# Performance work log

Hardware: AMD Instinct MI355X
Metric: run time of the kernel (lower is better)

## Reference

```python
import jax, jax.numpy as jnp
import numpy as np

# Dims: N tokens, top_k K, E experts, d_model D, expert hidden H
N, K, E, D, H = 4096, 2, 8, 1024, 1024


def setup_inputs() -> dict:
    key = jax.random.key(0)
    k1, k2, k3, k4, k5, k6 = jax.random.split(key, 6)
    x = jax.random.normal(k1, (N, D), dtype=jnp.float32)
    expert_indices = jax.random.randint(k2, (N, K), 0, E, dtype=jnp.int32)
    ew = jax.random.uniform(k3, (N, K), dtype=jnp.float32)
    expert_weights = ew / ew.sum(-1, keepdims=True)  # router probs over top-k
    # histogram consistent with expert_indices (computed by the router in the real model)
    batch_size_per_expert = jnp.bincount(expert_indices.reshape(-1), length=E).astype(jnp.int32)
    w1 = jax.random.normal(k4, (E, D, H), dtype=jnp.float32) * (D ** -0.5)
    w3 = jax.random.normal(k5, (E, D, H), dtype=jnp.float32) * (D ** -0.5)
    w2 = jax.random.normal(k6, (E, H, D), dtype=jnp.float32) * (H ** -0.5)
    return {
        "x": x,
        "expert_weights": expert_weights,
        "expert_indices": expert_indices,
        "batch_size_per_expert": batch_size_per_expert,
        "w1": w1,
        "w2": w2,
        "w3": w3,
    }


def reference(x, expert_weights, expert_indices, batch_size_per_expert, w1, w2, w3):
    """Dropless MoE: sort token-copies by expert, grouped-GEMM SwiGLU, unpermute+combine."""
    nk = N * K
    flat_idx = expert_indices.reshape(nk)               # (N*K,)
    order = jnp.argsort(flat_idx)                        # stable sort -> permutation into expert order
    x_perm = x[order // K]                               # (N*K, D) gather source token per copy
    gs = batch_size_per_expert.astype(jnp.int32)         # grouped-GEMM group sizes, sums to N*K
    # per-expert SwiGLU MLP via grouped GEMM (rows of x_perm are contiguous per expert)
    h = jax.nn.silu(jax.lax.ragged_dot(x_perm, w1, gs)) * jax.lax.ragged_dot(x_perm, w3, gs)  # (N*K, H)
    out_perm = jax.lax.ragged_dot(h, w2, gs)             # (N*K, D)
    # unpermute: scatter rows back to original (token, k) order
    out_flat = jnp.zeros_like(x_perm).at[order].set(out_perm)  # (N*K, D)
    # weighted combine over top-k copies
    out = jnp.einsum("nk,nkd->nd", expert_weights, out_flat.reshape(N, K, D))
    return out
```

## Files before the change

### kernel.cpp

```cpp
#include <hip/hip_runtime.h>
#include <hip/hip_bf16.h>
#include <stdint.h>

#define N_TOK   4096
#define TOPK    2
#define N_EXP   8
#define D_MODEL 1024
#define H_DIM   1024
#define NK      (N_TOK * TOPK)
#define MAX_TILES 72

typedef __attribute__((ext_vector_type(8))) short bf16x8;
typedef __attribute__((ext_vector_type(4))) float f32x4;
typedef __attribute__((ext_vector_type(4))) unsigned int uint32x4;
typedef __attribute__((ext_vector_type(2))) unsigned int uint32x2;
typedef unsigned short bfbits;

__device__ inline bfbits f2bf_bits(float f) {
  union { float f; unsigned int u; } v; v.f = f;
  unsigned int r = v.u + 0x7FFFu + ((v.u >> 16) & 1u);
  return (bfbits)(r >> 16);
}
__device__ inline float bf2f(unsigned short u) {
  union { unsigned int u; float f; } v; v.u = ((unsigned int)u) << 16;
  return v.f;
}

__device__ inline void glds16(const bfbits* g, bfbits* l) {
  __builtin_amdgcn_global_load_lds(
      (const __attribute__((address_space(1))) void*)g,
      (__attribute__((address_space(3))) void*)l, 16, 0, 0);
}

__global__ __launch_bounds__(256, 4) void prepass_kernel(
    const float* __restrict__ x, const int* __restrict__ eidx,
    const int* __restrict__ bspe,
    const float* __restrict__ w1, const float* __restrict__ w2,
    const float* __restrict__ w3,
    bfbits* __restrict__ w1t, bfbits* __restrict__ w2t,
    bfbits* __restrict__ w3t, bfbits* __restrict__ xb,
    int* __restrict__ meta, int* __restrict__ row_src,
    int* __restrict__ pos_of) {
  int z = blockIdx.z;
  int tid = threadIdx.x;

  if (z >= 1 && z <= 24) {
    int zz = z - 1;
    const size_t MAT = (size_t)1024 * 1024;
    const float* src; bfbits* dst;
    if (zz < 8)       { src = w1 + (size_t)zz * MAT;        dst = w1t + (size_t)zz * MAT; }
    else if (zz < 16) { src = w3 + (size_t)(zz - 8) * MAT;  dst = w3t + (size_t)(zz - 8) * MAT; }
    else              { src = w2 + (size_t)(zz - 16) * MAT; dst = w2t + (size_t)(zz - 16) * MAT; }

    __shared__ __align__(16) bfbits Ts[64 * 132];
    char* tsb = (char*)Ts;

    int r0 = blockIdx.y * 128, c0 = blockIdx.x * 64;
    int k = tid & 15, qw = tid >> 4;
    int c = k * 4;

    float4 v0[4], v1[4];
#pragma unroll
    for (int it = 0; it < 4; it++) {
      int r = it * 32 + qw * 2;
      v0[it] = *(const float4*)&src[(size_t)(r0 + r) * 1024 + c0 + c];
      v1[it] = *(const float4*)&src[(size_t)(r0 + r + 1) * 1024 + c0 + c];
    }
#pragma unroll
    for (int it = 0; it < 4; it++) {
      int r = it * 32 + qw * 2;
      const float* a0 = (const float*)&v0[it];
      const float* a1 = (const float*)&v1[it];
#pragma unroll
      for (int j = 0; j < 4; j++) {
        int a = c + j;
        int xo = ((a >> 4) & 3) << 3;
        unsigned int pk = (unsigned int)f2bf_bits(a0[j]) |
                          ((unsigned int)f2bf_bits(a1[j]) << 16);
        *(unsigned int*)(tsb + a * 264 + ((r * 2) ^ xo)) = pk;
      }
    }
    __syncthreads();
    int g = tid >> 3, m = tid & 7;
#pragma unroll
    for (int it2 = 0; it2 < 2; it2++) {
      int o = it2 * 32 + g;
      int base = o * 264;
      int xo = ((o >> 4) & 3) << 3;
      uint32x2 p0 = *(const uint32x2*)(tsb + base + ((m * 32 +  0) ^ xo));
      uint32x2 p1 = *(const uint32x2*)(tsb + base + ((m * 32 +  8) ^ xo));
      uint32x2 p2 = *(const uint32x2*)(tsb + base + ((m * 32 + 16) ^ xo));
      uint32x2 p3 = *(const uint32x2*)(tsb + base + ((m * 32 + 24) ^ xo));
      size_t ob = (size_t)(c0 + o) * 1024 + r0 + m * 16;
      uint32x4 s0; s0.x = p0.x; s0.y = p0.y; s0.z = p1.x; s0.w = p1.y;
      uint32x4 s1; s1.x = p2.x; s1.y = p2.y; s1.z = p3.x; s1.w = p3.y;
      *(uint32x4*)&dst[ob] = s0;
      *(uint32x4*)&dst[ob + 8] = s1;
    }
  } else if (z >= 25) {
    int idx = (z - 25) * 128 + blockIdx.y * 16 + blockIdx.x;
    const float4* xv = (const float4*)x;
    ushort4* xo = (ushort4*)xb;
#pragma unroll
    for (int q = 0; q < 4; q++) {
      int fi = idx * 1024 + q * 256 + tid;
      float4 v = xv[fi];
      ushort4 o;
      o.x = f2bf_bits(v.x); o.y = f2bf_bits(v.y);
      o.z = f2bf_bits(v.z); o.w = f2bf_bits(v.w);
      xo[fi] = o;
    }
  } else {
    if (blockIdx.x != 0 || blockIdx.y != 0) return;
    __shared__ int sm[162];
    __shared__ int scnt[N_EXP];
    if (tid == 0) {
      int acc = 0, nt = 0;
      for (int e = 0; e < N_EXP; e++) {
        sm[e] = acc;
        int g = bspe[e];
        for (int tt = 0; tt * 128 < g; tt++) {
          sm[18 + nt] = e;
          sm[90 + nt] = acc + tt * 128;
          nt++;
        }
        acc += g;
      }
      sm[8] = acc;
      sm[17] = nt;
      for (int i = nt; i < MAX_TILES; i++) { sm[18 + i] = 0; sm[90 + i] = 0; }
    }
    if (tid < N_EXP) scnt[tid] = 0;
    __syncthreads();
    int4 eb[8];
#pragma unroll
    for (int q = 0; q < 8; q++) eb[q] = ((const int4*)eidx)[q * 256 + tid];
#pragma unroll
    for (int q = 0; q < 8; q++) {
      int ii = (q * 256 + tid) * 4;
      const int* ev = (const int*)&eb[q];
#pragma unroll
      for (int j = 0; j < 4; j++) {
        int e = ev[j];
        int p = sm[e] + atomicAdd(&scnt[e], 1);
        row_src[p] = ii + j;
        pos_of[ii + j] = p;
      }
    }
    if (tid < 162) meta[tid] = sm[tid];
  }
}

__global__ __launch_bounds__(256, 3) void gemm_swiglu_kernel(
    const bfbits* __restrict__ xb, const bfbits* __restrict__ w1t,
    const bfbits* __restrict__ w3t, const int* __restrict__ row_src,
    const int* __restrict__ meta, bfbits* __restrict__ hb) {
  int nt = meta[17];
  int bt = blockIdx.y;
  if (bt >= nt) return;
  int e = meta[18 + bt];
  int row0 = meta[90 + bt];
  int rows_end = meta[e + 1];
  int n0 = blockIdx.x * 64;

  __shared__ __align__(16) bfbits As[128 * 64];
  __shared__ __align__(16) bfbits B1s[64 * 64];
  __shared__ __align__(16) bfbits B3s[64 * 64];

  int tid = threadIdx.x, lane = tid & 63, wv = tid >> 6;
  int r8 = lane >> 3, jl = lane & 7;
  int jg = jl ^ r8;

  const bfbits* gp[8]; bfbits* lp[8];
  for (int j = 0; j < 8; j++) {
    int s = wv * 8 + j;
    if (s < 16) {
      int tok = row_src[row0 + s * 8 + r8] >> 1;
      gp[j] = xb + (size_t)tok * D_MODEL + jg * 8;
      lp[j] = As + s * 512;
    } else if (s < 24) {
      int b = s - 16;
      gp[j] = w1t + ((size_t)e * H_DIM + n0 + b * 8 + r8) * D_MODEL + jg * 8;
      lp[j] = B1s + b * 512;
    } else {
      int b = s - 24;
      gp[j] = w3t + ((size_t)e * H_DIM + n0 + b * 8 + r8) * D_MODEL + jg * 8;
      lp[j] = B3s + b * 512;
    }
  }

  const f32x4 fzero = {0.f, 0.f, 0.f, 0.f};
  f32x4 accg[4][2], accu[4][2];
  for (int i = 0; i < 4; i++)
    for (int j = 0; j < 2; j++) { accg[i][j] = fzero; accu[i][j] = fzero; }

  int mw = (wv & 1) * 64, nwv = (wv >> 1) * 32;
  int qd = lane >> 4, lr = lane & 15, lr7 = lr & 7;

  for (int kk = 0; kk < D_MODEL / 64; kk++) {
    int ko = kk * 64;
    for (int j = 0; j < 8; j++) glds16(gp[j] + ko, lp[j]);
    __syncthreads();
    for (int ks = 0; ks < 2; ks++) {
      int sb = ((ks * 4 + qd) ^ lr7) << 3;
      bf16x8 af[4], b1f[2], b3f[2];
      for (int mi = 0; mi < 4; mi++)
        af[mi] = *(const bf16x8*)&As[(mw + mi * 16 + lr) * 64 + sb];
      for (int ni = 0; ni < 2; ni++) {
        b1f[ni] = *(const bf16x8*)&B1s[(nwv + ni * 16 + lr) * 64 + sb];
        b3f[ni] = *(const bf16x8*)&B3s[(nwv + ni * 16 + lr) * 64 + sb];
      }
      for (int mi = 0; mi < 4; mi++)
        for (int ni = 0; ni < 2; ni++) {
          accg[mi][ni] = __builtin_amdgcn_mfma_f32_16x16x32_bf16(af[mi], b1f[ni], accg[mi][ni], 0, 0, 0);
          accu[mi][ni] = __builtin_amdgcn_mfma_f32_16x16x32_bf16(af[mi], b3f[ni], accu[mi][ni], 0, 0, 0);
        }
    }
    __syncthreads();
  }

  for (int mi = 0; mi < 4; mi++) {
    int rbase = row0 + mw + mi * 16 + qd * 4;
    for (int r = 0; r < 4; r++) {
      int grow = rbase + r;
      if (grow < rows_end) {
        for (int ni = 0; ni < 2; ni++) {
          float gg = accg[mi][ni][r], u = accu[mi][ni][r];
          float h = gg / (1.f + __expf(-gg)) * u;
          hb[(size_t)grow * H_DIM + n0 + nwv + ni * 16 + lr] = f2bf_bits(h);
        }
      }
    }
  }
}

__global__ __launch_bounds__(256, 2) void gemm_out_kernel(
    const bfbits* __restrict__ hb, const bfbits* __restrict__ w2t,
    const int* __restrict__ meta, bfbits* __restrict__ out_perm) {
  int nt = meta[17];
  int bt = blockIdx.y;
  if (bt >= nt) return;
  int e = meta[18 + bt];
  int row0 = meta[90 + bt];
  int rows_end = meta[e + 1];
  int n0 = blockIdx.x * 128;

  __shared__ __align__(16) bfbits As[128 * 64];
  __shared__ __align__(16) bfbits Bs[128 * 64];

  int tid = threadIdx.x, lane = tid & 63, wv = tid >> 6;
  int r8 = lane >> 3, jl = lane & 7;
  int jg = jl ^ r8;

  const bfbits* gp[8]; bfbits* lp[8];
  for (int j = 0; j < 8; j++) {
    int s = wv * 8 + j;
    if (s < 16) {
      gp[j] = hb + (size_t)(row0 + s * 8 + r8) * H_DIM + jg * 8;
      lp[j] = As + s * 512;
    } else {
      int b = s - 16;
      gp[j] = w2t + ((size_t)e * D_MODEL + n0 + b * 8 + r8) * H_DIM + jg * 8;
      lp[j] = Bs + b * 512;
    }
  }

  const f32x4 fzero = {0.f, 0.f, 0.f, 0.f};
  f32x4 acc[4][4];
  for (int i = 0; i < 4; i++)
    for (int j = 0; j < 4; j++) acc[i][j] = fzero;

  int mw = (wv & 1) * 64, nw = (wv >> 1) * 64;
  int qd = lane >> 4, lr = lane & 15, lr7 = lr & 7;

  for (int kk = 0; kk < H_DIM / 64; kk++) {
    int ko = kk * 64;
    for (int j = 0; j < 8; j++) glds16(gp[j] + ko, lp[j]);
    __syncthreads();
    for (int ks = 0; ks < 2; ks++) {
      int sb = ((ks * 4 + qd) ^ lr7) << 3;
      bf16x8 af[4], bfr[4];
      for (int mi = 0; mi < 4; mi++)
        af[mi] = *(const bf16x8*)&As[(mw + mi * 16 + lr) * 64 + sb];
      for (int ni = 0; ni < 4; ni++)
        bfr[ni] = *(const bf16x8*)&Bs[(nw + ni * 16 + lr) * 64 + sb];
      for (int mi = 0; mi < 4; mi++)
        for (int ni = 0; ni < 4; ni++)
          acc[mi][ni] = __builtin_amdgcn_mfma_f32_16x16x32_bf16(af[mi], bfr[ni], acc[mi][ni], 0, 0, 0);
    }
    __syncthreads();
  }

  for (int mi = 0; mi < 4; mi++) {
    int rbase = row0 + mw + mi * 16 + qd * 4;
    for (int r = 0; r < 4; r++) {
      int grow = rbase + r;
      if (grow < rows_end) {
        for (int ni = 0; ni < 4; ni++)
          out_perm[(size_t)grow * D_MODEL + n0 + nw + ni * 16 + lr] = f2bf_bits(acc[mi][ni][r]);
      }
    }
  }
}

__global__ __launch_bounds__(256) void combine_kernel(
    const ushort4* __restrict__ out_perm, const int* __restrict__ pos_of,
    const float* __restrict__ ew, float4* __restrict__ out) {
  int tid = threadIdx.x;
#pragma unroll
  for (int q = 0; q < 4; q++) {
    int i = blockIdx.x * 1024 + q * 256 + tid;
    int tok = i >> 8;
    int col = i & 255;
    int p0 = pos_of[2 * tok], p1 = pos_of[2 * tok + 1];
    float w0 = ew[2 * tok], w1 = ew[2 * tok + 1];
    ushort4 a = out_perm[(size_t)p0 * 256 + col];
    ushort4 b = out_perm[(size_t)p1 * 256 + col];
    float4 o;
    o.x = w0 * bf2f(a.x) + w1 * bf2f(b.x);
    o.y = w0 * bf2f(a.y) + w1 * bf2f(b.y);
    o.z = w0 * bf2f(a.z) + w1 * bf2f(b.z);
    o.w = w0 * bf2f(a.w) + w1 * bf2f(b.w);
    out[i] = o;
  }
}

extern "C" void kernel_launch(void* const* d_in, const int* in_sizes, int n_in,
                              void* d_out, int out_size, void* d_ws, size_t ws_size,
                              hipStream_t stream) {
  const float* x  = (const float*)d_in[0];
  const float* ew = (const float*)d_in[1];
  const int* eidx = (const int*)d_in[2];
  const int* bspe = (const int*)d_in[3];
  const float* w1 = (const float*)d_in[4];
  const float* w2 = (const float*)d_in[5];
  const float* w3 = (const float*)d_in[6];
  float* out = (float*)d_out;

  char* ws = (char*)d_ws;
  const size_t MB = 1024 * 1024;
  bfbits* w1t   = (bfbits*)(ws);
  bfbits* w3t   = (bfbits*)(ws + 16 * MB);
  bfbits* w2t   = (bfbits*)(ws + 32 * MB);
  bfbits* xb    = (bfbits*)(ws + 48 * MB);
  bfbits* hb    = (bfbits*)(ws + 56 * MB);
  bfbits* out_perm = (bfbits*)(ws);
  int* row_src  = (int*)(ws + 72 * MB);
  int* pos_of   = (int*)(ws + 72 * MB + 32 * 1024);
  int* meta     = (int*)(ws + 72 * MB + 64 * 1024);

  prepass_kernel<<<dim3(16, 8, 33), 256, 0, stream>>>(
      x, eidx, bspe, w1, w2, w3, w1t, w2t, w3t, xb, meta, row_src, pos_of);
  gemm_swiglu_kernel<<<dim3(H_DIM / 64, MAX_TILES), 256, 0, stream>>>(
      xb, w1t, w3t, row_src, meta, hb);
  gemm_out_kernel<<<dim3(D_MODEL / 128, MAX_TILES), 256, 0, stream>>>(
      hb, w2t, meta, out_perm);
  combine_kernel<<<(N_TOK * D_MODEL / 4) / 1024, 256, 0, stream>>>(
      (const ushort4*)out_perm, pos_of, ew, (float4*)out);
}
```

Before: 240.1 us.

## Double-buffer LDS tiles in both expert GEMMs to overlap loads with MFMA

Both grouped-GEMM kernels switch from a single shared-memory tile to two ping-pong buffers. The global-to-LDS loads for the next K step are issued before the MFMAs on the current buffer, with an explicit vmcnt drain and barrier between steps. MFMA blocks are wrapped in s_setprio, and the inner loops are fully unrolled. This hides global load latency behind compute, but it doubles LDS use, so the SwiGLU kernel's launch bound drops from 3 to 2 blocks per CU and occupancy may fall.

```diff
diff --git a/kernel.cpp b/kernel.cpp
--- a/kernel.cpp
+++ b/kernel.cpp
@@ -31,6 +31,11 @@
       (const __attribute__((address_space(1))) void*)g,
       (__attribute__((address_space(3))) void*)l, 16, 0, 0);
 }
+
+#define DRAIN_BAR() do {                                   \
+    asm volatile("s_waitcnt vmcnt(0)" ::: "memory");       \
+    __builtin_amdgcn_s_barrier();                          \
+  } while (0)
 
 __global__ __launch_bounds__(256, 4) void prepass_kernel(
     const float* __restrict__ x, const int* __restrict__ eidx,
@@ -151,7 +156,7 @@
   }
 }
 
-__global__ __launch_bounds__(256, 3) void gemm_swiglu_kernel(
+__global__ __launch_bounds__(256, 2) void gemm_swiglu_kernel(
     const bfbits* __restrict__ xb, const bfbits* __restrict__ w1t,
     const bfbits* __restrict__ w3t, const int* __restrict__ row_src,
     const int* __restrict__ meta, bfbits* __restrict__ hb) {
@@ -163,29 +168,30 @@
   int rows_end = meta[e + 1];
   int n0 = blockIdx.x * 64;
 
-  __shared__ __align__(16) bfbits As[128 * 64];
-  __shared__ __align__(16) bfbits B1s[64 * 64];
-  __shared__ __align__(16) bfbits B3s[64 * 64];
+  __shared__ __align__(16) bfbits sA[2][128 * 64];
+  __shared__ __align__(16) bfbits sB1[2][64 * 64];
+  __shared__ __align__(16) bfbits sB3[2][64 * 64];
 
   int tid = threadIdx.x, lane = tid & 63, wv = tid >> 6;
   int r8 = lane >> 3, jl = lane & 7;
   int jg = jl ^ r8;
 
-  const bfbits* gp[8]; bfbits* lp[8];
+  const bfbits* gp[8]; bfbits* lp0[8]; bfbits* lp1[8];
+#pragma unroll
   for (int j = 0; j < 8; j++) {
     int s = wv * 8 + j;
     if (s < 16) {
       int tok = row_src[row0 + s * 8 + r8] >> 1;
       gp[j] = xb + (size_t)tok * D_MODEL + jg * 8;
-      lp[j] = As + s * 512;
+      lp0[j] = &sA[0][s * 512];  lp1[j] = &sA[1][s * 512];
     } else if (s < 24) {
       int b = s - 16;
       gp[j] = w1t + ((size_t)e * H_DIM + n0 + b * 8 + r8) * D_MODEL + jg * 8;
-      lp[j] = B1s + b * 512;
+      lp0[j] = &sB1[0][b * 512]; lp1[j] = &sB1[1][b * 512];
     } else {
       int b = s - 24;
       gp[j] = w3t + ((size_t)e * H_DIM + n0 + b * 8 + r8) * D_MODEL + jg * 8;
-      lp[j] = B3s + b * 512;
+      lp0[j] = &sB3[0][b * 512]; lp1[j] = &sB3[1][b * 512];
     }
   }
 
@@ -197,27 +203,50 @@
   int mw = (wv & 1) * 64, nwv = (wv >> 1) * 32;
   int qd = lane >> 4, lr = lane & 15, lr7 = lr & 7;
 
-  for (int kk = 0; kk < D_MODEL / 64; kk++) {
-    int ko = kk * 64;
-    for (int j = 0; j < 8; j++) glds16(gp[j] + ko, lp[j]);
-    __syncthreads();
+  auto compute = [&](const bfbits* As, const bfbits* B1s, const bfbits* B3s) {
+#pragma unroll
     for (int ks = 0; ks < 2; ks++) {
       int sb = ((ks * 4 + qd) ^ lr7) << 3;
       bf16x8 af[4], b1f[2], b3f[2];
+#pragma unroll
       for (int mi = 0; mi < 4; mi++)
         af[mi] = *(const bf16x8*)&As[(mw + mi * 16 + lr) * 64 + sb];
+#pragma unroll
       for (int ni = 0; ni < 2; ni++) {
         b1f[ni] = *(const bf16x8*)&B1s[(nwv + ni * 16 + lr) * 64 + sb];
         b3f[ni] = *(const bf16x8*)&B3s[(nwv + ni * 16 + lr) * 64 + sb];
       }
+      __builtin_amdgcn_s_setprio(1);
+#pragma unroll
       for (int mi = 0; mi < 4; mi++)
+#pragma unroll
         for (int ni = 0; ni < 2; ni++) {
           accg[mi][ni] = __builtin_amdgcn_mfma_f32_16x16x32_bf16(af[mi], b1f[ni], accg[mi][ni], 0, 0, 0);
           accu[mi][ni] = __builtin_amdgcn_mfma_f32_16x16x32_bf16(af[mi], b3f[ni], accu[mi][ni], 0, 0, 0);
         }
-    }
-    __syncthreads();
-  }
+      __builtin_amdgcn_s_setprio(0);
+    }
+  };
+
+#pragma unroll
+  for (int j = 0; j < 8; j++) glds16(gp[j], lp0[j]);
+  DRAIN_BAR();
+
+  for (int kk = 0; kk < 14; kk += 2) {
+#pragma unroll
+    for (int j = 0; j < 8; j++) glds16(gp[j] + (kk + 1) * 64, lp1[j]);
+    compute(sA[0], sB1[0], sB3[0]);
+    DRAIN_BAR();
+#pragma unroll
+    for (int j = 0; j < 8; j++) glds16(gp[j] + (kk + 2) * 64, lp0[j]);
+    compute(sA[1], sB1[1], sB3[1]);
+    DRAIN_BAR();
+  }
+#pragma unroll
+  for (int j = 0; j < 8; j++) glds16(gp[j] + 15 * 64, lp1[j]);
+  compute(sA[0], sB1[0], sB3[0]);
+  DRAIN_BAR();
+  compute(sA[1], sB1[1], sB3[1]);
 
   for (int mi = 0; mi < 4; mi++) {
     int rbase = row0 + mw + mi * 16 + qd * 4;
@@ -245,23 +274,24 @@
   int rows_end = meta[e + 1];
   int n0 = blockIdx.x * 128;
 
-  __shared__ __align__(16) bfbits As[128 * 64];
-  __shared__ __align__(16) bfbits Bs[128 * 64];
+  __shared__ __align__(16) bfbits sA[2][128 * 64];
+  __shared__ __align__(16) bfbits sB[2][128 * 64];
 
   int tid = threadIdx.x, lane = tid & 63, wv = tid >> 6;
   int r8 = lane >> 3, jl = lane & 7;
   int jg = jl ^ r8;
 
-  const bfbits* gp[8]; bfbits* lp[8];
+  const bfbits* gp[8]; bfbits* lp0[8]; bfbits* lp1[8];
+#pragma unroll
   for (int j = 0; j < 8; j++) {
     int s = wv * 8 + j;
     if (s < 16) {
       gp[j] = hb + (size_t)(row0 + s * 8 + r8) * H_DIM + jg * 8;
-      lp[j] = As + s * 512;
+      lp0[j] = &sA[0][s * 512];  lp1[j] = &sA[1][s * 512];
     } else {
       int b = s - 16;
       gp[j] = w2t + ((size_t)e * D_MODEL + n0 + b * 8 + r8) * H_DIM + jg * 8;
-      lp[j] = Bs + b * 512;
+      lp0[j] = &sB[0][b * 512];  lp1[j] = &sB[1][b * 512];
     }
   }
 
@@ -273,23 +303,46 @@
   int mw = (wv & 1) * 64, nw = (wv >> 1) * 64;
   int qd = lane >> 4, lr = lane & 15, lr7 = lr & 7;
 
-  for (int kk = 0; kk < H_DIM / 64; kk++) {
-    int ko = kk * 64;
-    for (int j = 0; j < 8; j++) glds16(gp[j] + ko, lp[j]);
-    __syncthreads();
+  auto compute = [&](const bfbits* As, const bfbits* Bs) {
+#pragma unroll
     for (int ks = 0; ks < 2; ks++) {
       int sb = ((ks * 4 + qd) ^ lr7) << 3;
       bf16x8 af[4], bfr[4];
+#pragma unroll
       for (int mi = 0; mi < 4; mi++)
         af[mi] = *(const bf16x8*)&As[(mw + mi * 16 + lr) * 64 + sb];
+#pragma unroll
       for (int ni = 0; ni < 4; ni++)
         bfr[ni] = *(const bf16x8*)&Bs[(nw + ni * 16 + lr) * 64 + sb];
+      __builtin_amdgcn_s_setprio(1);
+#pragma unroll
       for (int mi = 0; mi < 4; mi++)
+#pragma unroll
         for (int ni = 0; ni < 4; ni++)
           acc[mi][ni] = __builtin_amdgcn_mfma_f32_16x16x32_bf16(af[mi], bfr[ni], acc[mi][ni], 0, 0, 0);
-    }
-    __syncthreads();
-  }
+      __builtin_amdgcn_s_setprio(0);
+    }
+  };
+
+#pragma unroll
+  for (int j = 0; j < 8; j++) glds16(gp[j], lp0[j]);
+  DRAIN_BAR();
+
+  for (int kk = 0; kk < 14; kk += 2) {
+#pragma unroll
+    for (int j = 0; j < 8; j++) glds16(gp[j] + (kk + 1) * 64, lp1[j]);
+    compute(sA[0], sB[0]);
+    DRAIN_BAR();
+#pragma unroll
+    for (int j = 0; j < 8; j++) glds16(gp[j] + (kk + 2) * 64, lp0[j]);
+    compute(sA[1], sB[1]);
+    DRAIN_BAR();
+  }
+#pragma unroll
+  for (int j = 0; j < 8; j++) glds16(gp[j] + 15 * 64, lp1[j]);
+  compute(sA[0], sB[0]);
+  DRAIN_BAR();
+  compute(sA[1], sB[1]);
 
   for (int mi = 0; mi < 4; mi++) {
     int rbase = row0 + mw + mi * 16 + qd * 4;
```

After: 238.9 us. About the same (-0.5%).
